# Kernel tuning notes

Measured on AMD Instinct MI355X. Metric: run time of the kernel, lower is better.

Reference implementation:

```python
import jax, jax.numpy as jnp
import numpy as np

B, T, H, L = 256, 256, 768, 13
START, STOP = 11, 12
NEG = -10000.0


def setup_inputs() -> dict:
    key = jax.random.key(0)
    k1, k2, k3 = jax.random.split(key, 3)
    bert_seq_out = jax.random.normal(k1, (B, T, H), jnp.float32)
    W = jax.random.normal(k2, (L, H), jnp.float32) * 0.02  # hidden2label weight
    b = jnp.zeros((L,), jnp.float32)                        # hidden2label bias
    transitions = jax.random.normal(k3, (L, L), jnp.float32)
    transitions = transitions.at[START, :].set(NEG).at[:, STOP].set(NEG)
    return {"bert_seq_out": bert_seq_out, "W": W, "b": b, "transitions": transitions}


def _viterbi(feats, transitions):
    # feats: [B, T, L]
    Bn, Tn, Ln = feats.shape
    ld0 = jnp.full((Bn, Ln), NEG, feats.dtype).at[:, START].set(0.0)

    def step(ld, feat_t):
        # scores[b, to, from] = transitions[to, from] + ld[b, from]
        scores = transitions[None, :, :] + ld[:, None, :]
        psi_t = jnp.argmax(scores, axis=-1)            # [B, L] backpointers
        ld_new = jnp.max(scores, axis=-1) + feat_t     # [B, L]
        return ld_new, psi_t

    feats_t = jnp.swapaxes(feats, 0, 1)  # [T, B, L]
    ld_final, psi = jax.lax.scan(step, ld0, feats_t[1:])  # psi: [T-1, B, L]

    a = jax.nn.softmax(ld_final, axis=-1)  # matches F.softmax(log_delta) in torch
    max_p = jnp.max(a, axis=-1)            # [B]
    last = jnp.argmax(a, axis=-1)          # [B] final tag

    def back(nxt, psi_t):
        prev = jnp.take_along_axis(psi_t, nxt[:, None], axis=1)[:, 0]
        return prev, prev

    # reverse scan: path[t] = psi[t+1][b, path[t+1]] for t = T-2 .. 0
    _, path_prev = jax.lax.scan(back, last, psi, reverse=True)  # [T-1, B]
    path = jnp.concatenate([jnp.swapaxes(path_prev, 0, 1), last[:, None]], axis=1)  # [B, T]
    return (1.0 / Tn) * max_p, path


def reference(bert_seq_out, W, b, transitions):
    # dropout is identity at inference; hidden2label linear projection
    feats = jnp.einsum('bth,lh->btl', bert_seq_out, W) + b  # [B, T, L]
    return _viterbi(feats, transitions)
```

## Files before the change

### kernel.cpp

```cpp
#include <hip/hip_runtime.h>


#define NEGV (-10000.0f)

#define DPP_ADD(v, ctrl, rmask)                                               \
  v += __int_as_float(__builtin_amdgcn_update_dpp(                            \
      0, __float_as_int(v), (ctrl), (rmask), 0xF, true));

#define DPP_REDUCE64(v)                                                       \
  DPP_ADD(v, 0x111, 0xF)                                      \
  DPP_ADD(v, 0x112, 0xF)                                      \
  DPP_ADD(v, 0x114, 0xF)                                      \
  DPP_ADD(v, 0x118, 0xF)                                      \
  DPP_ADD(v, 0x142, 0xA)                                    \
  DPP_ADD(v, 0x143, 0xC)

__device__ __forceinline__ float vstep_asm(float ld, const float* tr, float ft) {
  float out, v0, v1, v2, v3, v4, v5;
  int s0, s1, s2, s3, s4, s5;
  asm("v_readlane_b32 %[s0], %[ld], 0\n\t"
      "v_readlane_b32 %[s1], %[ld], 1\n\t"
      "v_readlane_b32 %[s2], %[ld], 2\n\t"
      "v_readlane_b32 %[s3], %[ld], 3\n\t"
      "v_readlane_b32 %[s4], %[ld], 4\n\t"
      "v_readlane_b32 %[s5], %[ld], 5\n\t"
      "v_add_f32 %[v0], %[s0], %[t0]\n\t"
      "v_add_f32 %[v1], %[s1], %[t1]\n\t"
      "v_add_f32 %[v2], %[s2], %[t2]\n\t"
      "v_readlane_b32 %[s0], %[ld], 6\n\t"
      "v_readlane_b32 %[s1], %[ld], 7\n\t"
      "v_readlane_b32 %[s2], %[ld], 8\n\t"
      "v_add_f32 %[v3], %[s3], %[t3]\n\t"
      "v_add_f32 %[v4], %[s4], %[t4]\n\t"
      "v_add_f32 %[v5], %[s5], %[t5]\n\t"
      "v_max3_f32 %[v0], %[v0], %[v1], %[v2]\n\t"
      "v_max3_f32 %[v3], %[v3], %[v4], %[v5]\n\t"
      "v_readlane_b32 %[s3], %[ld], 9\n\t"
      "v_readlane_b32 %[s4], %[ld], 10\n\t"
      "v_readlane_b32 %[s5], %[ld], 11\n\t"
      "v_add_f32 %[v1], %[s0], %[t6]\n\t"
      "v_add_f32 %[v2], %[s1], %[t7]\n\t"
      "v_add_f32 %[v4], %[s2], %[t8]\n\t"
      "v_readlane_b32 %[s0], %[ld], 12\n\t"
      "v_max3_f32 %[v1], %[v1], %[v2], %[v4]\n\t"
      "v_add_f32 %[v2], %[s3], %[t9]\n\t"
      "v_add_f32 %[v4], %[s4], %[t10]\n\t"
      "v_add_f32 %[v5], %[s5], %[t11]\n\t"
      "v_max3_f32 %[v2], %[v2], %[v4], %[v5]\n\t"
      "v_add_f32 %[v4], %[s0], %[t12]\n\t"
      "v_max3_f32 %[v0], %[v0], %[v3], %[v1]\n\t"
      "v_max3_f32 %[v0], %[v0], %[v2], %[v4]\n\t"
      "v_add_f32 %[o], %[v0], %[ft]"
      : [o] "=&v"(out),
        [s0] "=&s"(s0), [s1] "=&s"(s1), [s2] "=&s"(s2),
        [s3] "=&s"(s3), [s4] "=&s"(s4), [s5] "=&s"(s5),
        [v0] "=&v"(v0), [v1] "=&v"(v1), [v2] "=&v"(v2),
        [v3] "=&v"(v3), [v4] "=&v"(v4), [v5] "=&v"(v5)
      : [ld] "v"(ld), [ft] "v"(ft),
        [t0] "v"(tr[0]), [t1] "v"(tr[1]), [t2] "v"(tr[2]), [t3] "v"(tr[3]),
        [t4] "v"(tr[4]), [t5] "v"(tr[5]), [t6] "v"(tr[6]), [t7] "v"(tr[7]),
        [t8] "v"(tr[8]), [t9] "v"(tr[9]), [t10] "v"(tr[10]),
        [t11] "v"(tr[11]), [t12] "v"(tr[12]));
  return out;
}

__global__ __launch_bounds__(512)
__attribute__((amdgpu_waves_per_eu(2, 2)))
void fused_kernel(
    const float* __restrict__ X,
    const float* __restrict__ W,
    const float* __restrict__ bias,
    const float* __restrict__ trans,
    float* __restrict__ out)
{
  __shared__ float fsT[13 * 260];
  __shared__ float lds_ld[256 * 16];
  __shared__ float trL[176];
  __shared__ unsigned char psi[256 * 16];
  __shared__ unsigned char Mm[256];
  __shared__ unsigned char bnd[16];
  __shared__ unsigned char path[256];
  __shared__ int flags[256];

  const int tid = threadIdx.x;
  const int w = tid >> 6, l = tid & 63;
  const int b = blockIdx.x;

  if (tid < 169) trL[tid] = trans[tid];
  if (tid < 256) flags[tid] = 0;
  __syncthreads();

  if (w == 0) {
    if (l < 16) {
      const int lane = l;
      float tr[13];
      #pragma unroll
      for (int f = 0; f < 13; ++f)
        tr[f] = (lane < 13) ? trans[lane * 13 + f] : -1.0e30f;

      const int toc = (lane < 13) ? lane : 0;
      const float* frow = &fsT[toc * 260];
      volatile int* vf = flags;

      float ld = (lane == 11) ? 0.0f : NEGV;
      lds_ld[lane] = ld;

      #pragma unroll 1
      for (int g = 0; g < 16; ++g) {
        while (!__all(vf[g * 16 + lane] != 0)) {}
        asm volatile("" ::: "memory");

        float4 F[4];
        #pragma unroll
        for (int q = 0; q < 4; ++q)
          F[q] = *reinterpret_cast<const float4*>(frow + g * 16 + 4 * q);

        if (g == 0) {
          #pragma unroll
          for (int k = 1; k < 16; ++k) {
            const float4 fq = F[k >> 2];
            const float ftv = ((k & 3) == 0) ? fq.x : ((k & 3) == 1) ? fq.y
                             : ((k & 3) == 2) ? fq.z : fq.w;
            ld = vstep_asm(ld, tr, ftv);
            lds_ld[k * 16 + lane] = ld;
          }
        } else {
          #pragma unroll
          for (int k = 0; k < 16; ++k) {
            const int t = g * 16 + k;
            const float4 fq = F[k >> 2];
            const float ftv = ((k & 3) == 0) ? fq.x : ((k & 3) == 1) ? fq.y
                             : ((k & 3) == 2) ? fq.z : fq.w;
            ld = vstep_asm(ld, tr, ftv);
            lds_ld[t * 16 + lane] = ld;
          }
        }
      }
    }
  } else {
    const int pw = w - 1;
    float wreg[13][12];
    #pragma unroll
    for (int col = 0; col < 13; ++col) {
      #pragma unroll
      for (int j = 0; j < 3; ++j) {
        float4 v = *reinterpret_cast<const float4*>(W + col * 768 + 256 * j + 4 * l);
        wreg[col][4 * j + 0] = v.x; wreg[col][4 * j + 1] = v.y;
        wreg[col][4 * j + 2] = v.z; wreg[col][4 * j + 3] = v.w;
      }
    }
    float bs[13];
    #pragma unroll
    for (int c = 0; c < 13; ++c) bs[c] = bias[c];

    const float* Xb = X + (long)b * 196608 + 4 * l;

    float4 buf[4][3];
    #pragma unroll
    for (int i = 0; i < 4; ++i) {
      const float* xr = Xb + (pw + 7 * i) * 768;
      buf[i][0] = *reinterpret_cast<const float4*>(xr);
      buf[i][1] = *reinterpret_cast<const float4*>(xr + 256);
      buf[i][2] = *reinterpret_cast<const float4*>(xr + 512);
    }

    #define PROW(i, s)                                                        \
    {                                                                         \
      const int r = pw + 7 * (i);                                             \
      const float4 b0 = buf[s][0], b1 = buf[s][1], b2 = buf[s][2];            \
      float acc[13];                                                          \
      _Pragma("unroll")                                                       \
      for (int c = 0; c < 13; ++c) acc[c] = 0.0f;                             \
      _Pragma("unroll")                                                       \
      for (int col = 0; col < 13; ++col) {                                    \
        acc[col] = fmaf(b0.x, wreg[col][0],  acc[col]);                       \
        acc[col] = fmaf(b0.y, wreg[col][1],  acc[col]);                       \
        acc[col] = fmaf(b0.z, wreg[col][2],  acc[col]);                       \
        acc[col] = fmaf(b0.w, wreg[col][3],  acc[col]);                       \
        acc[col] = fmaf(b1.x, wreg[col][4],  acc[col]);                       \
        acc[col] = fmaf(b1.y, wreg[col][5],  acc[col]);                       \
        acc[col] = fmaf(b1.z, wreg[col][6],  acc[col]);                       \
        acc[col] = fmaf(b1.w, wreg[col][7],  acc[col]);                       \
        acc[col] = fmaf(b2.x, wreg[col][8],  acc[col]);                       \
        acc[col] = fmaf(b2.y, wreg[col][9],  acc[col]);                       \
        acc[col] = fmaf(b2.z, wreg[col][10], acc[col]);                       \
        acc[col] = fmaf(b2.w, wreg[col][11], acc[col]);                       \
      }                                                                       \
      _Pragma("unroll")                                                       \
      for (int c = 0; c < 13; ++c) {                                          \
        DPP_REDUCE64(acc[c])                                                  \
      }                                                                       \
      if (l == 63) {                                                          \
        _Pragma("unroll")                                                     \
        for (int c = 0; c < 13; ++c)                                          \
          fsT[c * 260 + r] = acc[c] + bs[c];                                  \
        asm volatile("s_waitcnt lgkmcnt(0)" ::: "memory");                    \
        flags[r] = 1;                                                         \
      }                                                                       \
    }

    #pragma unroll 4
    for (int i = 0; i < 36; ++i) {
      const int s = i & 3;
      PROW(i, s)
      {
        const int rn = pw + 7 * (i + 4);
        const int rc = (rn < 256) ? rn : 255;
        const float* xn = Xb + rc * 768;
        buf[s][0] = *reinterpret_cast<const float4*>(xn);
        buf[s][1] = *reinterpret_cast<const float4*>(xn + 256);
        buf[s][2] = *reinterpret_cast<const float4*>(xn + 512);
      }
    }
    if (pw < 4) {
      PROW(36, 0)
    }
    #undef PROW
  }
  __syncthreads();

  {
    const int to = tid & 15, dtt = tid >> 4;
    if (to < 13) {
      float trr[13];
      #pragma unroll
      for (int f = 0; f < 13; ++f) trr[f] = trL[to * 13 + f];
      for (int t = (dtt == 0 ? 32 : dtt); t < 256; t += 32) {
        const float* lp = &lds_ld[(t - 1) * 16];
        float4 l0 = *reinterpret_cast<const float4*>(lp);
        float4 l1 = *reinterpret_cast<const float4*>(lp + 4);
        float4 l2 = *reinterpret_cast<const float4*>(lp + 8);
        float4 l3 = *reinterpret_cast<const float4*>(lp + 12);
        float c[13] = {trr[0] + l0.x,  trr[1] + l0.y,  trr[2] + l0.z,
                       trr[3] + l0.w,  trr[4] + l1.x,  trr[5] + l1.y,
                       trr[6] + l1.z,  trr[7] + l1.w,  trr[8] + l2.x,
                       trr[9] + l2.y,  trr[10] + l2.z, trr[11] + l2.w,
                       trr[12] + l3.x};
        float best = c[0]; int bf = 0;
        #pragma unroll
        for (int f = 1; f < 13; ++f) {
          bool gt = c[f] > best;
          best = gt ? c[f] : best;
          bf   = gt ? f : bf;
        }
        psi[t * 16 + to] = (unsigned char)bf;
      }
    }
  }
  __syncthreads();

  if (tid < 256) {
    const int sS = tid & 15, g = tid >> 4;
    if (sS < 13) {
      int cur = sS;
      const int tLo = (g == 0) ? 1 : g * 16;
      for (int t = g * 16 + 15; t >= tLo; --t)
        cur = psi[t * 16 + cur];
      Mm[g * 16 + sS] = (unsigned char)cur;
    }
  }
  __syncthreads();

  if (tid == 0) {
    const float* lf = &lds_ld[255 * 16];
    float m = lf[0]; int last = 0;
    #pragma unroll
    for (int i = 1; i < 13; ++i)
      if (lf[i] > m) { m = lf[i]; last = i; }
    float ssum = 0.0f;
    #pragma unroll
    for (int i = 0; i < 13; ++i) ssum += expf(lf[i] - m);
    out[b] = 1.0f / (256.0f * ssum);

    int cur = last;
    bnd[15] = (unsigned char)cur;
    #pragma unroll
    for (int cc = 15; cc >= 1; --cc) {
      cur = Mm[cc * 16 + cur];
      bnd[cc - 1] = (unsigned char)cur;
    }
  }
  __syncthreads();

  if (tid < 16) {
    int cur = bnd[tid];
    const int tHi = tid * 16 + 15;
    path[tHi] = (unsigned char)cur;
    const int tLo = (tid == 0) ? 1 : tid * 16;
    for (int t = tHi; t >= tLo; --t) {
      cur = psi[t * 16 + cur];
      path[t - 1] = (unsigned char)cur;
    }
  }
  __syncthreads();

  if (tid < 256)
    out[256 + (long)b * 256 + tid] = (float)path[tid];
}

extern "C" void kernel_launch(void* const* d_in, const int* in_sizes, int n_in,
                              void* d_out, int out_size, void* d_ws, size_t ws_size,
                              hipStream_t stream) {
  const float* X     = (const float*)d_in[0];
  const float* W     = (const float*)d_in[1];
  const float* bias  = (const float*)d_in[2];
  const float* trans = (const float*)d_in[3];
  float* out = (float*)d_out;

  fused_kernel<<<256, 512, 0, stream>>>(X, W, bias, trans, out);
}
```

Before: 54.66 us.

## Split projection weights into two column halves to cut register pressure

The producer waves no longer hold all 13×12 weight values in registers. They process rows in chunks of 8, first computing label columns 0-6 and then reloading X and computing columns 7-12, with a one-row-ahead prefetch in place of the 4-deep buffer. Flags are set only after the second half, so the Viterbi wave still sees complete rows. This is meant to lower VGPR use at the cost of reading X twice and reloading W each chunk. It also adds s_sleep to the consumer's spin-wait to reduce polling contention, which can add wake-up latency.

Measured after the change: 60.28 us. 10.3% more time.

```diff
diff --git a/kernel.cpp b/kernel.cpp
--- a/kernel.cpp
+++ b/kernel.cpp
@@ -14,6 +14,14 @@
   DPP_ADD(v, 0x118, 0xF)                                      \
   DPP_ADD(v, 0x142, 0xA)                                    \
   DPP_ADD(v, 0x143, 0xC)
+
+#define FMA_ROW(accv, wcol)                                                   \
+  accv = fmaf(x0.x, wcol[0],  accv); accv = fmaf(x0.y, wcol[1],  accv);       \
+  accv = fmaf(x0.z, wcol[2],  accv); accv = fmaf(x0.w, wcol[3],  accv);       \
+  accv = fmaf(x1.x, wcol[4],  accv); accv = fmaf(x1.y, wcol[5],  accv);       \
+  accv = fmaf(x1.z, wcol[6],  accv); accv = fmaf(x1.w, wcol[7],  accv);       \
+  accv = fmaf(x2.x, wcol[8],  accv); accv = fmaf(x2.y, wcol[9],  accv);       \
+  accv = fmaf(x2.z, wcol[10], accv); accv = fmaf(x2.w, wcol[11], accv);
 
 __device__ __forceinline__ float vstep_asm(float ld, const float* tr, float ft) {
   float out, v0, v1, v2, v3, v4, v5;
@@ -107,7 +115,9 @@
 
       #pragma unroll 1
       for (int g = 0; g < 16; ++g) {
-        while (!__all(vf[g * 16 + lane] != 0)) {}
+        while (!__all(vf[g * 16 + lane] != 0)) {
+          __builtin_amdgcn_s_sleep(1);
+        }
         asm volatile("" ::: "memory");
 
         float4 F[4];
@@ -139,83 +149,116 @@
     }
   } else {
     const int pw = w - 1;
-    float wreg[13][12];
-    #pragma unroll
-    for (int col = 0; col < 13; ++col) {
-      #pragma unroll
-      for (int j = 0; j < 3; ++j) {
-        float4 v = *reinterpret_cast<const float4*>(W + col * 768 + 256 * j + 4 * l);
-        wreg[col][4 * j + 0] = v.x; wreg[col][4 * j + 1] = v.y;
-        wreg[col][4 * j + 2] = v.z; wreg[col][4 * j + 3] = v.w;
-      }
-    }
+    const int imax = (pw < 4) ? 37 : 36;
+    const float* Xb = X + (long)b * 196608 + 4 * l;
+
     float bs[13];
     #pragma unroll
     for (int c = 0; c < 13; ++c) bs[c] = bias[c];
 
-    const float* Xb = X + (long)b * 196608 + 4 * l;
-
-    float4 buf[4][3];
-    #pragma unroll
-    for (int i = 0; i < 4; ++i) {
-      const float* xr = Xb + (pw + 7 * i) * 768;
-      buf[i][0] = *reinterpret_cast<const float4*>(xr);
-      buf[i][1] = *reinterpret_cast<const float4*>(xr + 256);
-      buf[i][2] = *reinterpret_cast<const float4*>(xr + 512);
-    }
-
-    #define PROW(i, s)                                                        \
-    {                                                                         \
-      const int r = pw + 7 * (i);                                             \
-      const float4 b0 = buf[s][0], b1 = buf[s][1], b2 = buf[s][2];            \
-      float acc[13];                                                          \
-      _Pragma("unroll")                                                       \
-      for (int c = 0; c < 13; ++c) acc[c] = 0.0f;                             \
-      _Pragma("unroll")                                                       \
-      for (int col = 0; col < 13; ++col) {                                    \
-        acc[col] = fmaf(b0.x, wreg[col][0],  acc[col]);                       \
-        acc[col] = fmaf(b0.y, wreg[col][1],  acc[col]);                       \
-        acc[col] = fmaf(b0.z, wreg[col][2],  acc[col]);                       \
-        acc[col] = fmaf(b0.w, wreg[col][3],  acc[col]);                       \
-        acc[col] = fmaf(b1.x, wreg[col][4],  acc[col]);                       \
-        acc[col] = fmaf(b1.y, wreg[col][5],  acc[col]);                       \
-        acc[col] = fmaf(b1.z, wreg[col][6],  acc[col]);                       \
-        acc[col] = fmaf(b1.w, wreg[col][7],  acc[col]);                       \
-        acc[col] = fmaf(b2.x, wreg[col][8],  acc[col]);                       \
-        acc[col] = fmaf(b2.y, wreg[col][9],  acc[col]);                       \
-        acc[col] = fmaf(b2.z, wreg[col][10], acc[col]);                       \
-        acc[col] = fmaf(b2.w, wreg[col][11], acc[col]);                       \
-      }                                                                       \
-      _Pragma("unroll")                                                       \
-      for (int c = 0; c < 13; ++c) {                                          \
-        DPP_REDUCE64(acc[c])                                                  \
-      }                                                                       \
-      if (l == 63) {                                                          \
-        _Pragma("unroll")                                                     \
-        for (int c = 0; c < 13; ++c)                                          \
-          fsT[c * 260 + r] = acc[c] + bs[c];                                  \
-        asm volatile("s_waitcnt lgkmcnt(0)" ::: "memory");                    \
-        flags[r] = 1;                                                         \
-      }                                                                       \
-    }
-
-    #pragma unroll 4
-    for (int i = 0; i < 36; ++i) {
-      const int s = i & 3;
-      PROW(i, s)
+    #pragma unroll 1
+    for (int ch = 0; ch < 5; ++ch) {
+      const int i0 = ch * 8;
+      if (i0 >= imax) break;
+
       {
-        const int rn = pw + 7 * (i + 4);
-        const int rc = (rn < 256) ? rn : 255;
-        const float* xn = Xb + rc * 768;
-        buf[s][0] = *reinterpret_cast<const float4*>(xn);
-        buf[s][1] = *reinterpret_cast<const float4*>(xn + 256);
-        buf[s][2] = *reinterpret_cast<const float4*>(xn + 512);
+        float wA[7][12];
+        #pragma unroll
+        for (int col = 0; col < 7; ++col) {
+          #pragma unroll
+          for (int j = 0; j < 3; ++j) {
+            float4 v = *reinterpret_cast<const float4*>(
+                W + col * 768 + 256 * j + 4 * l);
+            wA[col][4*j+0] = v.x; wA[col][4*j+1] = v.y;
+            wA[col][4*j+2] = v.z; wA[col][4*j+3] = v.w;
+          }
+        }
+        float4 x0, x1, x2, n0, n1, n2;
+        {
+          const float* xr = Xb + (pw + 7 * i0) * 768;
+          x0 = *reinterpret_cast<const float4*>(xr);
+          x1 = *reinterpret_cast<const float4*>(xr + 256);
+          x2 = *reinterpret_cast<const float4*>(xr + 512);
+        }
+        #pragma unroll
+        for (int j = 0; j < 8; ++j) {
+          const int i = i0 + j;
+          if (i < imax) {
+            {
+              const int inx = (i + 1 < imax) ? i + 1 : i;
+              const float* xr = Xb + (pw + 7 * inx) * 768;
+              n0 = *reinterpret_cast<const float4*>(xr);
+              n1 = *reinterpret_cast<const float4*>(xr + 256);
+              n2 = *reinterpret_cast<const float4*>(xr + 512);
+            }
+            float acc[7];
+            #pragma unroll
+            for (int c = 0; c < 7; ++c) acc[c] = 0.0f;
+            #pragma unroll
+            for (int c = 0; c < 7; ++c) { FMA_ROW(acc[c], wA[c]) }
+            #pragma unroll
+            for (int c = 0; c < 7; ++c) { DPP_REDUCE64(acc[c]) }
+            if (l == 63) {
+              const int r = pw + 7 * i;
+              #pragma unroll
+              for (int c = 0; c < 7; ++c)
+                fsT[c * 260 + r] = acc[c] + bs[c];
+            }
+            x0 = n0; x1 = n1; x2 = n2;
+          }
+        }
       }
-    }
-    if (pw < 4) {
-      PROW(36, 0)
-    }
-    #undef PROW
+
+      {
+        float wB[6][12];
+        #pragma unroll
+        for (int col = 0; col < 6; ++col) {
+          #pragma unroll
+          for (int j = 0; j < 3; ++j) {
+            float4 v = *reinterpret_cast<const float4*>(
+                W + (7 + col) * 768 + 256 * j + 4 * l);
+            wB[col][4*j+0] = v.x; wB[col][4*j+1] = v.y;
+            wB[col][4*j+2] = v.z; wB[col][4*j+3] = v.w;
+          }
+        }
+        float4 x0, x1, x2, n0, n1, n2;
+        {
+          const float* xr = Xb + (pw + 7 * i0) * 768;
+          x0 = *reinterpret_cast<const float4*>(xr);
+          x1 = *reinterpret_cast<const float4*>(xr + 256);
+          x2 = *reinterpret_cast<const float4*>(xr + 512);
+        }
+        #pragma unroll
+        for (int j = 0; j < 8; ++j) {
+          const int i = i0 + j;
+          if (i < imax) {
+            {
+              const int inx = (i + 1 < imax) ? i + 1 : i;
+              const float* xr = Xb + (pw + 7 * inx) * 768;
+              n0 = *reinterpret_cast<const float4*>(xr);
+              n1 = *reinterpret_cast<const float4*>(xr + 256);
+              n2 = *reinterpret_cast<const float4*>(xr + 512);
+            }
+            float acc[6];
+            #pragma unroll
+            for (int c = 0; c < 6; ++c) acc[c] = 0.0f;
+            #pragma unroll
+            for (int c = 0; c < 6; ++c) { FMA_ROW(acc[c], wB[c]) }
+            #pragma unroll
+            for (int c = 0; c < 6; ++c) { DPP_REDUCE64(acc[c]) }
+            if (l == 63) {
+              const int r = pw + 7 * i;
+              #pragma unroll
+              for (int c = 0; c < 6; ++c)
+                fsT[(7 + c) * 260 + r] = acc[c] + bs[7 + c];
+              asm volatile("s_waitcnt lgkmcnt(0)" ::: "memory");
+              flags[r] = 1;
+            }
+            x0 = n0; x1 = n1; x2 = n2;
+          }
+        }
+      }
+    }
   }
   __syncthreads();
 
```
